# Performance work log

Hardware: AMD Instinct MI355X
Metric: run time of the kernel (lower is better)

Reference implementation:

```python
import jax, jax.numpy as jnp
import numpy as np

B, S, H = 2, 2048, 2048
NQ, NKV = 32, 8          # query heads, kv heads
G = NQ // NKV            # query groups per kv head
D = H // NQ              # head dim = 64
MAX_POS = 4096
THETA = 10000.0


def _rope_tables(position_ids):
    # freqs per the original apply_rotary_emb (interleaved pair convention)
    freqs = 1.0 / THETA ** (jnp.arange(0, D, 2)[: D // 2].astype(jnp.float32) / D)
    t = jnp.arange(MAX_POS, dtype=jnp.float32)
    ang = jnp.outer(t, freqs)                     # [MAX_POS, D/2]
    cos = jnp.take(jnp.cos(ang), position_ids, axis=0)[:, :, None, :]  # [B,S,1,D/2]
    sin = jnp.take(jnp.sin(ang), position_ids, axis=0)[:, :, None, :]
    return cos, sin


def _apply_rope(x, cos, sin):
    # x: [B,S,h,D]; pairs are interleaved (x0,x1),(x2,x3),...
    x2 = x.astype(jnp.float32).reshape(*x.shape[:-1], D // 2, 2)
    xr, xi = x2[..., 0], x2[..., 1]
    out_r = xr * cos - xi * sin
    out_i = xr * sin + xi * cos
    return jnp.stack((out_r, out_i), axis=-1).reshape(x.shape).astype(x.dtype)


def setup_inputs() -> dict:
    key = jax.random.key(0)
    ks = jax.random.split(key, 5)
    init_scale = 0.02 / np.sqrt(H)
    hidden_states = jax.random.normal(ks[0], (B, S, H), dtype=jnp.float32)
    wq = jax.random.normal(ks[1], (H, H), dtype=jnp.float32) * init_scale
    wk = jax.random.normal(ks[2], (H, H // G), dtype=jnp.float32) * init_scale
    wv = jax.random.normal(ks[3], (H, H // G), dtype=jnp.float32) * init_scale
    wo = jax.random.normal(ks[4], (H, H), dtype=jnp.float32) * init_scale
    attention_mask = jnp.ones((B, S), dtype=jnp.int32)
    position_ids = jnp.broadcast_to(jnp.arange(S, dtype=jnp.int32), (B, S))
    return dict(hidden_states=hidden_states, attention_mask=attention_mask,
                position_ids=position_ids, wq=wq, wk=wk, wv=wv, wo=wo)


def reference(hidden_states, attention_mask, position_ids, wq, wk, wv, wo):
    # projections (no bias)
    xq = (hidden_states @ wq).reshape(B, S, NQ, D)
    xk = (hidden_states @ wk).reshape(B, S, NKV, D)
    xv = (hidden_states @ wv).reshape(B, S, NKV, D)
    # GQA repeat: kv head h -> query heads h*G .. h*G+G-1 (consecutive)
    xk = jnp.repeat(xk, G, axis=2)  # [B,S,NQ,D]
    xv = jnp.repeat(xv, G, axis=2)

    cos, sin = _rope_tables(position_ids)
    xq = _apply_rope(xq, cos, sin)
    xk = _apply_rope(xk, cos, sin)

    # causal + padding mask -> additive bias
    causal = jnp.tril(jnp.ones((S, S), dtype=bool))[None, None]          # [1,1,S,S]
    pad = (attention_mask > 0)[:, None, None, :]                          # [B,1,1,S]
    combined = jnp.logical_and(causal, pad)                               # [B,1,S,S]
    neg = jnp.finfo(jnp.float32).min
    bias = jnp.where(combined, 0.0, neg).astype(jnp.float32)

    scale = 1.0 / np.sqrt(D)
    scores = jnp.einsum('bqhd,bkhd->bhqk', xq, xk).astype(jnp.float32) * scale
    scores = scores + bias
    attn = jax.nn.softmax(scores, axis=-1)                                # [B,NQ,S,S] fp32
    out = jnp.einsum('bhqk,bkhd->bqhd', attn, xv)                         # [B,S,NQ,D]
    out = out.reshape(B, S, H)
    return out @ wo
```

## Files before the change

kernel.cpp:

```cpp
#include <hip/hip_runtime.h>
#include <cstdint>

typedef __attribute__((ext_vector_type(8))) __bf16  bf8v;
typedef __attribute__((ext_vector_type(4))) float   f4v;
typedef __attribute__((ext_vector_type(2))) float   f2v;
typedef __attribute__((ext_vector_type(4))) short   s4v;
typedef __attribute__((ext_vector_type(8))) unsigned short ush8;

__device__ __forceinline__ float bf2f(unsigned short u) {
    union { unsigned u; float f; } v; v.u = ((unsigned)u) << 16; return v.f;
}
__device__ __forceinline__ unsigned short f2bf_n(float f) {
    union { __bf16 h; unsigned short s; } v; v.h = (__bf16)f; return v.s;
}
__device__ __forceinline__ unsigned pack2bf(float a, float b) {
    union { __bf16 h[2]; unsigned u; } v;
    v.h[0] = (__bf16)a; v.h[1] = (__bf16)b; return v.u;
}

#define GLDS16(gp, lp)                                                          \
    __builtin_amdgcn_global_load_lds(                                           \
        (const __attribute__((address_space(1))) void*)(uintptr_t)(gp),         \
        (__attribute__((address_space(3))) void*)(uintptr_t)(lp), 16, 0, 0)

__global__ void cast_f32_to_bf16(const float* __restrict__ in,
                                 unsigned short* __restrict__ out, int n8) {
    int i = blockIdx.x * 256 + threadIdx.x;
    if (i >= n8) return;
    float4 a = ((const float4*)in)[2 * i];
    float4 b = ((const float4*)in)[2 * i + 1];
    uint4 o;
    o.x = pack2bf(a.x, a.y);
    o.y = pack2bf(a.z, a.w);
    o.z = pack2bf(b.x, b.y);
    o.w = pack2bf(b.z, b.w);
    ((uint4*)out)[i] = o;
}

__global__ void transpose_cast(const float* __restrict__ in,
                               unsigned short* __restrict__ out, int R, int C) {
    __shared__ float t[32][33];
    int c0 = blockIdx.x * 32, r0 = blockIdx.y * 32;
    int x = threadIdx.x, y = threadIdx.y;
    #pragma unroll
    for (int i = 0; i < 32; i += 8) t[y + i][x] = in[(size_t)(r0 + y + i) * C + c0 + x];
    __syncthreads();
    #pragma unroll
    for (int i = 0; i < 32; i += 8)
        out[(size_t)(c0 + y + i) * R + r0 + x] = f2bf_n(t[x][y + i]);
}

__global__ void transpose_v_bf16(const unsigned short* __restrict__ in,
                                 unsigned short* __restrict__ out) {
    __shared__ unsigned short t[32][33];
    int c0 = blockIdx.x * 32;
    int r0 = blockIdx.y * 32;
    int x = threadIdx.x, y = threadIdx.y;
    #pragma unroll
    for (int i = 0; i < 32; i += 8)
        t[y + i][x] = in[(size_t)(r0 + y + i) * 3072 + 2560 + c0 + x];
    __syncthreads();
    #pragma unroll
    for (int i = 0; i < 32; i += 8) {
        int d   = c0 + y + i;
        int tok = r0 + x;
        int g   = (tok >> 2) & 15;
        int tp  = (tok & ~63) | (((g ^ (d & 15)) << 2)) | (tok & 3);
        out[(size_t)d * 4096 + tp] = t[x][y + i];
    }
}

__global__ void rope_strided(unsigned short* __restrict__ X,
                             const int* __restrict__ pos_ids,
                             int coloff, int stride, int nh_log2) {
    int idx = blockIdx.x * 256 + threadIdx.x;
    int i   = idx & 31;
    int hh  = (idx >> 5) & ((1 << nh_log2) - 1);
    int tok = idx >> (5 + nh_log2);
    int pos = pos_ids[tok];
    float ang = (float)pos * exp2f(-0.41524101186092f * (float)i);
    float s = sinf(ang), c = cosf(ang);
    unsigned short* p = X + (size_t)tok * stride + coloff + hh * 64 + 2 * i;
    unsigned pr = *(const unsigned*)p;
    float xr = bf2f((unsigned short)(pr & 0xffff));
    float xi = bf2f((unsigned short)(pr >> 16));
    float orr = xr * c - xi * s;
    float oi  = xr * s + xi * c;
    *(unsigned*)p = pack2bf(orr, oi);
}

template <int OUT_BF16>
__global__ __launch_bounds__(256) void gemm_bt(const unsigned short* __restrict__ A,
                                               const unsigned short* __restrict__ Bt,
                                               void* __restrict__ Cv, int N, int K) {
    __shared__ __align__(16) unsigned short As[128 * 64];
    __shared__ __align__(16) unsigned short Bs[128 * 64];
    const int t = threadIdx.x;
    const int lane = t & 63, w = t >> 6;
    const int wr = w >> 1, wc = w & 1;
    const int lr = lane & 15, lh = lane >> 4;
    const int m0 = blockIdx.y * 128, n0 = blockIdx.x * 128;

    f4v acc[4][4];
    #pragma unroll
    for (int i = 0; i < 4; ++i)
        #pragma unroll
        for (int j = 0; j < 4; ++j) acc[i][j] = f4v{0.f, 0.f, 0.f, 0.f};

    const int o_t = t * 16;
    for (int k0 = 0; k0 < K; k0 += 64) {
        __syncthreads();
        #pragma unroll
        for (int s = 0; s < 4; ++s) {
            int o = s * 4096 + o_t;
            int row = o >> 7;
            int src = (o & 127) ^ ((row & 7) << 4);
            const unsigned short* gA = A + (size_t)(m0 + row) * K + k0 + (src >> 1);
            GLDS16(gA, As + (o >> 1));
            const unsigned short* gB = Bt + (size_t)(n0 + row) * K + k0 + (src >> 1);
            GLDS16(gB, Bs + (o >> 1));
        }
        __syncthreads();
        #pragma unroll
        for (int kk = 0; kk < 2; ++kk) {
            bf8v af[4], bfr[4];
            #pragma unroll
            for (int mi = 0; mi < 4; ++mi) {
                int row = wr * 64 + mi * 16 + lr;
                int col = (kk * 32 + lh * 8) ^ ((row & 7) << 3);
                af[mi] = *(const bf8v*)(As + row * 64 + col);
            }
            #pragma unroll
            for (int ni = 0; ni < 4; ++ni) {
                int row = wc * 64 + ni * 16 + lr;
                int col = (kk * 32 + lh * 8) ^ ((row & 7) << 3);
                bfr[ni] = *(const bf8v*)(Bs + row * 64 + col);
            }
            #pragma unroll
            for (int mi = 0; mi < 4; ++mi)
                #pragma unroll
                for (int ni = 0; ni < 4; ++ni)
                    acc[mi][ni] = __builtin_amdgcn_mfma_f32_16x16x32_bf16(
                        af[mi], bfr[ni], acc[mi][ni], 0, 0, 0);
        }
    }
    #pragma unroll
    for (int mi = 0; mi < 4; ++mi)
        #pragma unroll
        for (int ni = 0; ni < 4; ++ni)
            #pragma unroll
            for (int r = 0; r < 4; ++r) {
                int row = m0 + wr * 64 + mi * 16 + lh * 4 + r;
                int col = n0 + wc * 64 + ni * 16 + lr;
                float v = acc[mi][ni][r];
                if (OUT_BF16) ((unsigned short*)Cv)[(size_t)row * N + col] = f2bf_n(v);
                else          ((float*)Cv)[(size_t)row * N + col] = v;
            }
}

__global__ __launch_bounds__(256, 4) void flash_attn(
        const unsigned short* __restrict__ QKV,
        const unsigned short* __restrict__ VtG,
        const int* __restrict__ amask,
        const int* __restrict__ pos_ids,
        unsigned short* __restrict__ O) {
    __shared__ __align__(16) unsigned short Ks[2][64 * 64];
    __shared__ __align__(16) unsigned short Vs[2][64 * 64];

    const int t = threadIdx.x, lane = t & 63, w = t >> 6;
    const int lr = lane & 15, lh = lane >> 4;
    const int pair = blockIdx.x, h = blockIdx.y, b = blockIdx.z;
    const size_t tok0 = (size_t)b * 2048;

    const unsigned short* Kb = QKV + tok0 * 3072 + 2048 + (h >> 2) * 64;
    const unsigned short* Vb = VtG + (size_t)((h >> 2) * 64) * 4096 + tok0;
    const int* amrow = amask + b * 2048;

#define STAGE(buf, kt)                                                              \
    {   _Pragma("unroll")                                                           \
        for (int s_ = 0; s_ < 2; ++s_) {                                            \
            int c_ = s_ * 256 + t;                                                  \
            int row_ = c_ >> 3;                                                     \
            int sc_ = (((c_ & 7) * 16) ^ ((row_ & 7) << 4)) >> 1;                   \
            GLDS16(Kb + (size_t)((kt) * 64 + row_) * 3072 + sc_, Ks[buf] + c_ * 8); \
            GLDS16(Vb + (size_t)row_ * 4096 + (kt) * 64 + (c_ & 7) * 8,             \
                   Vs[buf] + c_ * 8);                                               \
        }                                                                           \
    }

    const float SCL = 0.18033688011112042f;

    unsigned aliveMaskV = 0;
    {
        const int4* am4 = (const int4*)amrow;
        #pragma unroll
        for (int s = 0; s < 8; ++s) {
            int4 a = am4[s * 64 + lane];
            unsigned long long bal = __ballot(a.x && a.y && a.z && a.w);
            #pragma unroll
            for (int g = 0; g < 4; ++g)
                aliveMaskV |= (((bal >> (16 * g)) & 0xFFFFull) == 0xFFFFull)
                                  ? (1u << (4 * s + g)) : 0u;
        }
    }
    const int aliveMask = __builtin_amdgcn_readfirstlane((int)aliveMaskV);

    int vcol[4];
    #pragma unroll
    for (int kf = 0; kf < 4; ++kf) vcol[kf] = ((kf * 4 + lh) ^ lr) * 4;

    int cur = 0;
    STAGE(cur, 0);

    #pragma unroll 1
    for (int half = 0; half < 2; ++half) {
        const int qt = half ? (31 - pair) : pair;
        const int q0 = qt * 64;
        const int qloc = w * 16 + lr;

        const unsigned short* Qp = QKV + (tok0 + q0 + qloc) * 3072 + h * 64;
        union Q8 { bf8v v; unsigned short s[8]; } qa0u, qa1u;
        qa0u.v = *(const bf8v*)(Qp + lh * 8);
        qa1u.v = *(const bf8v*)(Qp + 32 + lh * 8);
        {
            int pos = pos_ids[tok0 + q0 + qloc];
            #pragma unroll
            for (int r = 0; r < 4; ++r) {
                float i0 = (float)(lh * 4 + r);
                float ang0 = (float)pos * exp2f(-0.41524101186092f * i0);
                float sn = sinf(ang0), cs = cosf(ang0);
                float xr = bf2f(qa0u.s[2 * r]), xi = bf2f(qa0u.s[2 * r + 1]);
                qa0u.s[2 * r]     = f2bf_n((xr * cs - xi * sn) * SCL);
                qa0u.s[2 * r + 1] = f2bf_n((xr * sn + xi * cs) * SCL);
                float i1 = (float)(16 + lh * 4 + r);
                float ang1 = (float)pos * exp2f(-0.41524101186092f * i1);
                float sn1 = sinf(ang1), cs1 = cosf(ang1);
                float yr = bf2f(qa1u.s[2 * r]), yi = bf2f(qa1u.s[2 * r + 1]);
                qa1u.s[2 * r]     = f2bf_n((yr * cs1 - yi * sn1) * SCL);
                qa1u.s[2 * r + 1] = f2bf_n((yr * sn1 + yi * cs1) * SCL);
            }
        }
        const bf8v qa0 = qa0u.v, qa1 = qa1u.v;

        f4v oacc[4];
        #pragma unroll
        for (int i = 0; i < 4; ++i) oacc[i] = f4v{0.f, 0.f, 0.f, 0.f};
        float m_ = -1e30f, l_ = 0.f;
        f4v sa[4];

        auto qk = [&](int curb) {
            #pragma unroll
            for (int kf = 0; kf < 4; ++kf) sa[kf] = f4v{0.f, 0.f, 0.f, 0.f};
            __builtin_amdgcn_s_setprio(1);
            #pragma unroll
            for (int kk = 0; kk < 2; ++kk) {
                bf8v qa = kk ? qa1 : qa0;
                int col = kk * 32 + lh * 8;
                #pragma unroll
                for (int kf = 0; kf < 4; ++kf) {
                    bf8v kb = *(const bf8v*)(Ks[curb] + (kf * 16 + lr) * 64 + (col ^ ((lr & 7) << 3)));
                    sa[kf] = __builtin_amdgcn_mfma_f32_16x16x32_bf16(kb, qa, sa[kf], 0, 0, 0);
                }
            }
            __builtin_amdgcn_s_setprio(0);
        };

        auto softmax_pv = [&](int curb) {
            float pe[4][4];
            float rs;
            #pragma unroll 1
            for (;;) {
                #pragma unroll
                for (int kf = 0; kf < 4; ++kf)
                    #pragma unroll
                    for (int r = 0; r < 4; ++r)
                        pe[kf][r] = exp2f(sa[kf][r] - m_);
                f2v v0 = f2v{pe[0][0], pe[0][1]} + f2v{pe[0][2], pe[0][3]};
                f2v v1 = f2v{pe[1][0], pe[1][1]} + f2v{pe[1][2], pe[1][3]};
                f2v v2 = f2v{pe[2][0], pe[2][1]} + f2v{pe[2][2], pe[2][3]};
                f2v v3 = f2v{pe[3][0], pe[3][1]} + f2v{pe[3][2], pe[3][3]};
                f2v vv = (v0 + v1) + (v2 + v3);
                rs = vv[0] + vv[1];
                rs += __shfl_xor(rs, 16);
                rs += __shfl_xor(rs, 32);
                if (__builtin_expect(!__any(rs > 16777216.0f), 1)) break;
                float t0 = fmaxf(fmaxf(sa[0][0], sa[0][1]), fmaxf(sa[0][2], sa[0][3]));
                float t1 = fmaxf(fmaxf(sa[1][0], sa[1][1]), fmaxf(sa[1][2], sa[1][3]));
                float t2 = fmaxf(fmaxf(sa[2][0], sa[2][1]), fmaxf(sa[2][2], sa[2][3]));
                float t3 = fmaxf(fmaxf(sa[3][0], sa[3][1]), fmaxf(sa[3][2], sa[3][3]));
                float mx = fmaxf(fmaxf(t0, t1), fmaxf(t2, t3));
                mx = fmaxf(mx, __shfl_xor(mx, 16));
                mx = fmaxf(mx, __shfl_xor(mx, 32));
                float mn = fmaxf(m_, mx);
                float fac = exp2f(m_ - mn);
                m_ = mn;
                l_ *= fac;
                float facr[4];
                #pragma unroll
                for (int r = 0; r < 4; ++r) facr[r] = __shfl(fac, lh * 4 + r);
                #pragma unroll
                for (int df = 0; df < 4; ++df) {
                    f4v o = oacc[df];
                    o[0] *= facr[0]; o[1] *= facr[1]; o[2] *= facr[2]; o[3] *= facr[3];
                    oacc[df] = o;
                }
            }
            l_ += rs;
            __builtin_amdgcn_s_setprio(1);
            #pragma unroll
            for (int kf = 0; kf < 4; ++kf) {
                union { uint2 u; s4v s; } pa;
                pa.u.x = pack2bf(pe[kf][0], pe[kf][1]);
                pa.u.y = pack2bf(pe[kf][2], pe[kf][3]);
                #pragma unroll
                for (int df = 0; df < 4; ++df) {
                    const s4v vb = *(const s4v*)(Vs[curb] + (df * 16 + lr) * 64 + vcol[kf]);
                    oacc[df] = __builtin_amdgcn_mfma_f32_16x16x16bf16_1k(
                        pa.s, vb, oacc[df], 0, 0, 0);
                }
            }
            __builtin_amdgcn_s_setprio(0);
        };

        __syncthreads();

        #pragma unroll 1
        for (int kt = 0; kt < qt; ++kt) {
            STAGE(cur ^ 1, kt + 1);
            qk(cur);
            if (!((aliveMask >> kt) & 1)) {
                #pragma unroll
                for (int kf = 0; kf < 4; ++kf) {
                    int4 aq = *(const int4*)(amrow + kt * 64 + kf * 16 + lh * 4);
                    if (aq.x == 0) sa[kf][0] = -1e30f;
                    if (aq.y == 0) sa[kf][1] = -1e30f;
                    if (aq.z == 0) sa[kf][2] = -1e30f;
                    if (aq.w == 0) sa[kf][3] = -1e30f;
                }
            }
            softmax_pv(cur);
            __syncthreads();
            cur ^= 1;
        }

        if (half == 0) STAGE(cur ^ 1, 0);
        qk(cur);
        {
            const bool tileAlive = ((aliveMask >> qt) & 1) != 0;
            if (tileAlive) {
                #pragma unroll
                for (int kf = 0; kf < 4; ++kf)
                    #pragma unroll
                    for (int r = 0; r < 4; ++r) {
                        int keyl = kf * 16 + lh * 4 + r;
                        if (keyl > qloc) sa[kf][r] = -1e30f;
                    }
            } else {
                #pragma unroll
                for (int kf = 0; kf < 4; ++kf) {
                    int4 aq = *(const int4*)(amrow + qt * 64 + kf * 16 + lh * 4);
                    #pragma unroll
                    for (int r = 0; r < 4; ++r) {
                        int keyl = kf * 16 + lh * 4 + r;
                        int am = r == 0 ? aq.x : r == 1 ? aq.y : r == 2 ? aq.z : aq.w;
                        if (am == 0 || keyl > qloc) sa[kf][r] = -1e30f;
                    }
                }
            }
        }
        softmax_pv(cur);
        __syncthreads();
        cur ^= 1;

        float invl = 1.0f / l_;
        float invr[4];
        #pragma unroll
        for (int r = 0; r < 4; ++r) invr[r] = __shfl(invl, lh * 4 + r);
        #pragma unroll
        for (int df = 0; df < 4; ++df)
            #pragma unroll
            for (int r = 0; r < 4; ++r) {
                int qg = q0 + w * 16 + lh * 4 + r;
                float v = oacc[df][r] * invr[r];
                O[(tok0 + qg) * 2048 + h * 64 + df * 16 + lr] = f2bf_n(v);
            }
    }
#undef STAGE
}

extern "C" void kernel_launch(void* const* d_in, const int* in_sizes, int n_in,
                              void* d_out, int out_size, void* d_ws, size_t ws_size,
                              hipStream_t stream) {
    const float* hs   = (const float*)d_in[0];
    const int* amask  = (const int*)d_in[1];
    const int* pos    = (const int*)d_in[2];
    const float* wq   = (const float*)d_in[3];
    const float* wk   = (const float*)d_in[4];
    const float* wv   = (const float*)d_in[5];
    const float* wo   = (const float*)d_in[6];

    char* ws = (char*)d_ws;
    unsigned short* Xb   = (unsigned short*)(ws);
    unsigned short* Wqkv = (unsigned short*)(ws + 16777216);
    unsigned short* Wot  = (unsigned short*)(ws + 29360128);
    unsigned short* AOb  = (unsigned short*)(ws + 37748736);

    char* ob = (char*)d_out;
    unsigned short* QKV = (unsigned short*)ob;
    unsigned short* VtG = (unsigned short*)(ob + 25165824);

    cast_f32_to_bf16<<<4096, 256, 0, stream>>>(hs, Xb, 1048576);
    transpose_cast<<<dim3(64, 64), dim3(32, 8), 0, stream>>>(wq, Wqkv, 2048, 2048);
    transpose_cast<<<dim3(16, 64), dim3(32, 8), 0, stream>>>(wk, Wqkv + 4194304, 2048, 512);
    transpose_cast<<<dim3(16, 64), dim3(32, 8), 0, stream>>>(wv, Wqkv + 5242880, 2048, 512);
    transpose_cast<<<dim3(64, 64), dim3(32, 8), 0, stream>>>(wo, Wot, 2048, 2048);

    gemm_bt<1><<<dim3(24, 32), 256, 0, stream>>>(Xb, Wqkv, (void*)QKV, 3072, 2048);

    rope_strided<<<4096, 256, 0, stream>>>(QKV, pos, 2048, 3072, 3);

    transpose_v_bf16<<<dim3(16, 128), dim3(32, 8), 0, stream>>>(QKV, VtG);

    flash_attn<<<dim3(16, 32, 2), 256, 0, stream>>>(QKV, VtG, amask, pos, AOb);

    gemm_bt<0><<<dim3(16, 32), 256, 0, stream>>>(AOb, Wot, d_out, 2048, 2048);
}
```

Measured before the change: 225.4 us.

## Skip online-softmax max tracking when a global score bound guarantees safe exp

The RoPE kernel now also computes a global max-abs over all rotated K values with a wave reduction and an atomicMax. Flash attention uses that bound with the per-row Q max to prove the scores cannot overflow exp2. In that case it skips the running-max rescale loop and takes exp2 of the raw scores. The row sum is moved onto the MFMA unit by multiplying P by a ones matrix. The cost is an atomic per wave in RoPE, a memset, and an extra MFMA per key fragment. The general path is kept as a fallback.

```diff
diff --git a/kernel.cpp b/kernel.cpp
--- a/kernel.cpp
+++ b/kernel.cpp
@@ -72,7 +72,8 @@
 
 __global__ void rope_strided(unsigned short* __restrict__ X,
                              const int* __restrict__ pos_ids,
-                             int coloff, int stride, int nh_log2) {
+                             int coloff, int stride, int nh_log2,
+                             unsigned* __restrict__ kmax_out) {
     int idx = blockIdx.x * 256 + threadIdx.x;
     int i   = idx & 31;
     int hh  = (idx >> 5) & ((1 << nh_log2) - 1);
@@ -87,6 +88,10 @@
     float orr = xr * c - xi * s;
     float oi  = xr * s + xi * c;
     *(unsigned*)p = pack2bf(orr, oi);
+    float loc = fmaxf(fabsf(orr), fabsf(oi));
+    #pragma unroll
+    for (int off = 1; off < 64; off <<= 1) loc = fmaxf(loc, __shfl_xor(loc, off));
+    if ((threadIdx.x & 63) == 0) atomicMax(kmax_out, __float_as_uint(loc));
 }
 
 template <int OUT_BF16>
@@ -163,6 +168,7 @@
         const unsigned short* __restrict__ VtG,
         const int* __restrict__ amask,
         const int* __restrict__ pos_ids,
+        const unsigned* __restrict__ kmaxp,
         unsigned short* __restrict__ O) {
     __shared__ __align__(16) unsigned short Ks[2][64 * 64];
     __shared__ __align__(16) unsigned short Vs[2][64 * 64];
@@ -175,6 +181,7 @@
     const unsigned short* Kb = QKV + tok0 * 3072 + 2048 + (h >> 2) * 64;
     const unsigned short* Vb = VtG + (size_t)((h >> 2) * 64) * 4096 + tok0;
     const int* amrow = amask + b * 2048;
+    const float kmax = __uint_as_float(*kmaxp);
 
 #define STAGE(buf, kt)                                                              \
     {   _Pragma("unroll")                                                           \
@@ -189,6 +196,7 @@
     }
 
     const float SCL = 0.18033688011112042f;
+    const s4v ones = s4v{16256, 16256, 16256, 16256};
 
     unsigned aliveMaskV = 0;
     {
@@ -222,6 +230,7 @@
         union Q8 { bf8v v; unsigned short s[8]; } qa0u, qa1u;
         qa0u.v = *(const bf8v*)(Qp + lh * 8);
         qa1u.v = *(const bf8v*)(Qp + 32 + lh * 8);
+        float qrmax = 0.f;
         {
             int pos = pos_ids[tok0 + q0 + qloc];
             #pragma unroll
@@ -230,22 +239,30 @@
                 float ang0 = (float)pos * exp2f(-0.41524101186092f * i0);
                 float sn = sinf(ang0), cs = cosf(ang0);
                 float xr = bf2f(qa0u.s[2 * r]), xi = bf2f(qa0u.s[2 * r + 1]);
-                qa0u.s[2 * r]     = f2bf_n((xr * cs - xi * sn) * SCL);
-                qa0u.s[2 * r + 1] = f2bf_n((xr * sn + xi * cs) * SCL);
+                float a0 = (xr * cs - xi * sn) * SCL, a1 = (xr * sn + xi * cs) * SCL;
+                qa0u.s[2 * r]     = f2bf_n(a0);
+                qa0u.s[2 * r + 1] = f2bf_n(a1);
                 float i1 = (float)(16 + lh * 4 + r);
                 float ang1 = (float)pos * exp2f(-0.41524101186092f * i1);
                 float sn1 = sinf(ang1), cs1 = cosf(ang1);
                 float yr = bf2f(qa1u.s[2 * r]), yi = bf2f(qa1u.s[2 * r + 1]);
-                qa1u.s[2 * r]     = f2bf_n((yr * cs1 - yi * sn1) * SCL);
-                qa1u.s[2 * r + 1] = f2bf_n((yr * sn1 + yi * cs1) * SCL);
+                float b0 = (yr * cs1 - yi * sn1) * SCL, b1 = (yr * sn1 + yi * cs1) * SCL;
+                qa1u.s[2 * r]     = f2bf_n(b0);
+                qa1u.s[2 * r + 1] = f2bf_n(b1);
+                qrmax = fmaxf(qrmax, fmaxf(fmaxf(fabsf(a0), fabsf(a1)),
+                                           fmaxf(fabsf(b0), fabsf(b1))));
             }
         }
         const bf8v qa0 = qa0u.v, qa1 = qa1u.v;
+        qrmax = fmaxf(qrmax, __shfl_xor(qrmax, 16));
+        qrmax = fmaxf(qrmax, __shfl_xor(qrmax, 32));
+        const bool safe = __all(64.0f * qrmax * kmax * 1.02f < 80.0f);
 
         f4v oacc[4];
         #pragma unroll
         for (int i = 0; i < 4; ++i) oacc[i] = f4v{0.f, 0.f, 0.f, 0.f};
-        float m_ = -1e30f, l_ = 0.f;
+        f4v lacc = f4v{0.f, 0.f, 0.f, 0.f};
+        float m_ = 0.f;
         f4v sa[4];
 
         auto qk = [&](int curb) {
@@ -265,53 +282,14 @@
             __builtin_amdgcn_s_setprio(0);
         };
 
-        auto softmax_pv = [&](int curb) {
-            float pe[4][4];
-            float rs;
-            #pragma unroll 1
-            for (;;) {
-                #pragma unroll
-                for (int kf = 0; kf < 4; ++kf)
-                    #pragma unroll
-                    for (int r = 0; r < 4; ++r)
-                        pe[kf][r] = exp2f(sa[kf][r] - m_);
-                f2v v0 = f2v{pe[0][0], pe[0][1]} + f2v{pe[0][2], pe[0][3]};
-                f2v v1 = f2v{pe[1][0], pe[1][1]} + f2v{pe[1][2], pe[1][3]};
-                f2v v2 = f2v{pe[2][0], pe[2][1]} + f2v{pe[2][2], pe[2][3]};
-                f2v v3 = f2v{pe[3][0], pe[3][1]} + f2v{pe[3][2], pe[3][3]};
-                f2v vv = (v0 + v1) + (v2 + v3);
-                rs = vv[0] + vv[1];
-                rs += __shfl_xor(rs, 16);
-                rs += __shfl_xor(rs, 32);
-                if (__builtin_expect(!__any(rs > 16777216.0f), 1)) break;
-                float t0 = fmaxf(fmaxf(sa[0][0], sa[0][1]), fmaxf(sa[0][2], sa[0][3]));
-                float t1 = fmaxf(fmaxf(sa[1][0], sa[1][1]), fmaxf(sa[1][2], sa[1][3]));
-                float t2 = fmaxf(fmaxf(sa[2][0], sa[2][1]), fmaxf(sa[2][2], sa[2][3]));
-                float t3 = fmaxf(fmaxf(sa[3][0], sa[3][1]), fmaxf(sa[3][2], sa[3][3]));
-                float mx = fmaxf(fmaxf(t0, t1), fmaxf(t2, t3));
-                mx = fmaxf(mx, __shfl_xor(mx, 16));
-                mx = fmaxf(mx, __shfl_xor(mx, 32));
-                float mn = fmaxf(m_, mx);
-                float fac = exp2f(m_ - mn);
-                m_ = mn;
-                l_ *= fac;
-                float facr[4];
-                #pragma unroll
-                for (int r = 0; r < 4; ++r) facr[r] = __shfl(fac, lh * 4 + r);
-                #pragma unroll
-                for (int df = 0; df < 4; ++df) {
-                    f4v o = oacc[df];
-                    o[0] *= facr[0]; o[1] *= facr[1]; o[2] *= facr[2]; o[3] *= facr[3];
-                    oacc[df] = o;
-                }
-            }
-            l_ += rs;
+        auto pv = [&](int curb, float pe[4][4]) {
             __builtin_amdgcn_s_setprio(1);
             #pragma unroll
             for (int kf = 0; kf < 4; ++kf) {
                 union { uint2 u; s4v s; } pa;
                 pa.u.x = pack2bf(pe[kf][0], pe[kf][1]);
                 pa.u.y = pack2bf(pe[kf][2], pe[kf][3]);
+                lacc = __builtin_amdgcn_mfma_f32_16x16x16bf16_1k(pa.s, ones, lacc, 0, 0, 0);
                 #pragma unroll
                 for (int df = 0; df < 4; ++df) {
                     const s4v vb = *(const s4v*)(Vs[curb] + (df * 16 + lr) * 64 + vcol[kf]);
@@ -320,6 +298,57 @@
                 }
             }
             __builtin_amdgcn_s_setprio(0);
+        };
+
+        auto softmax_pv = [&](int curb) {
+            float pe[4][4];
+            if (__builtin_expect(safe, 1)) {
+                #pragma unroll
+                for (int kf = 0; kf < 4; ++kf)
+                    #pragma unroll
+                    for (int r = 0; r < 4; ++r)
+                        pe[kf][r] = exp2f(sa[kf][r]);
+            } else {
+                #pragma unroll 1
+                for (;;) {
+                    #pragma unroll
+                    for (int kf = 0; kf < 4; ++kf)
+                        #pragma unroll
+                        for (int r = 0; r < 4; ++r)
+                            pe[kf][r] = exp2f(sa[kf][r] - m_);
+                    f2v v0 = f2v{pe[0][0], pe[0][1]} + f2v{pe[0][2], pe[0][3]};
+                    f2v v1 = f2v{pe[1][0], pe[1][1]} + f2v{pe[1][2], pe[1][3]};
+                    f2v v2 = f2v{pe[2][0], pe[2][1]} + f2v{pe[2][2], pe[2][3]};
+                    f2v v3 = f2v{pe[3][0], pe[3][1]} + f2v{pe[3][2], pe[3][3]};
+                    f2v vv = (v0 + v1) + (v2 + v3);
+                    float rs = vv[0] + vv[1];
+                    rs += __shfl_xor(rs, 16);
+                    rs += __shfl_xor(rs, 32);
+                    if (!__any(rs > 16777216.0f)) break;
+                    float t0 = fmaxf(fmaxf(sa[0][0], sa[0][1]), fmaxf(sa[0][2], sa[0][3]));
+                    float t1 = fmaxf(fmaxf(sa[1][0], sa[1][1]), fmaxf(sa[1][2], sa[1][3]));
+                    float t2 = fmaxf(fmaxf(sa[2][0], sa[2][1]), fmaxf(sa[2][2], sa[2][3]));
+                    float t3 = fmaxf(fmaxf(sa[3][0], sa[3][1]), fmaxf(sa[3][2], sa[3][3]));
+                    float mx = fmaxf(fmaxf(t0, t1), fmaxf(t2, t3));
+                    mx = fmaxf(mx, __shfl_xor(mx, 16));
+                    mx = fmaxf(mx, __shfl_xor(mx, 32));
+                    float mn = fmaxf(m_, mx);
+                    float fac = exp2f(m_ - mn);
+                    m_ = mn;
+                    float facr[4];
+                    #pragma unroll
+                    for (int r = 0; r < 4; ++r) facr[r] = __shfl(fac, lh * 4 + r);
+                    lacc[0] *= facr[0]; lacc[1] *= facr[1];
+                    lacc[2] *= facr[2]; lacc[3] *= facr[3];
+                    #pragma unroll
+                    for (int df = 0; df < 4; ++df) {
+                        f4v o = oacc[df];
+                        o[0] *= facr[0]; o[1] *= facr[1]; o[2] *= facr[2]; o[3] *= facr[3];
+                        oacc[df] = o;
+                    }
+                }
+            }
+            pv(curb, pe);
         };
 
         __syncthreads();
@@ -372,10 +401,9 @@
         __syncthreads();
         cur ^= 1;
 
-        float invl = 1.0f / l_;
         float invr[4];
         #pragma unroll
-        for (int r = 0; r < 4; ++r) invr[r] = __shfl(invl, lh * 4 + r);
+        for (int r = 0; r < 4; ++r) invr[r] = 1.0f / lacc[r];
         #pragma unroll
         for (int df = 0; df < 4; ++df)
             #pragma unroll
@@ -404,6 +432,7 @@
     unsigned short* Wqkv = (unsigned short*)(ws + 16777216);
     unsigned short* Wot  = (unsigned short*)(ws + 29360128);
     unsigned short* AOb  = (unsigned short*)(ws + 37748736);
+    unsigned* kmaxp      = (unsigned*)(ws);
 
     char* ob = (char*)d_out;
     unsigned short* QKV = (unsigned short*)ob;
@@ -417,11 +446,13 @@
 
     gemm_bt<1><<<dim3(24, 32), 256, 0, stream>>>(Xb, Wqkv, (void*)QKV, 3072, 2048);
 
-    rope_strided<<<4096, 256, 0, stream>>>(QKV, pos, 2048, 3072, 3);
+    hipMemsetAsync(kmaxp, 0, 4, stream);
+
+    rope_strided<<<4096, 256, 0, stream>>>(QKV, pos, 2048, 3072, 3, kmaxp);
 
     transpose_v_bf16<<<dim3(16, 128), dim3(32, 8), 0, stream>>>(QKV, VtG);
 
-    flash_attn<<<dim3(16, 32, 2), 256, 0, stream>>>(QKV, VtG, amask, pos, AOb);
+    flash_attn<<<dim3(16, 32, 2), 256, 0, stream>>>(QKV, VtG, amask, pos, kmaxp, AOb);
 
     gemm_bt<0><<<dim3(16, 32), 256, 0, stream>>>(AOb, Wot, d_out, 2048, 2048);
 }
```

Result: slower. 400.2 us (+77.5%).
